# Performance work log

Hardware: AMD Instinct MI355X
Metric: run time of the kernel (lower is better)

## Reference

```python
import jax, jax.numpy as jnp
import numpy as np

B = 64        # number of graphs
NPG = 4096    # nodes per graph (equal-size segments, batch ids sorted)
H = 256       # hidden_dim
C0, C1 = 256, 64  # num_clusters


def setup_inputs() -> dict:
    key = jax.random.key(0)
    ks = jax.random.split(key, 8)
    N = B * NPG
    x = jax.random.normal(ks[0], (N, H), dtype=jnp.float32)
    edge_index = jax.random.randint(ks[1], (2, N), 0, N, dtype=jnp.int64)  # unused by forward
    batch = jnp.repeat(jnp.arange(B, dtype=jnp.int64), NPG)  # sorted, equal-size segments
    s = 1.0 / np.sqrt(H)
    W0 = jax.random.uniform(ks[2], (H, C0), jnp.float32, -s, s)
    b0 = jax.random.uniform(ks[3], (C0,), jnp.float32, -s, s)
    W1 = jax.random.uniform(ks[4], (H, C1), jnp.float32, -s, s)
    b1 = jax.random.uniform(ks[5], (C1,), jnp.float32, -s, s)
    sf = 1.0 / np.sqrt(C1 * H)
    Wf = jax.random.uniform(ks[6], (C1 * H, H), jnp.float32, -sf, sf)
    bf = jax.random.uniform(ks[7], (H,), jnp.float32, -sf, sf)
    return {"x": x, "edge_index": edge_index, "batch": batch,
            "W0": W0, "b0": b0, "W1": W1, "b1": b1, "Wf": Wf, "bf": bf}


def reference(x, edge_index, batch, W0, b0, W1, b1, Wf, bf):
    # Level 0: softmax cluster assignment + per-graph segmented matmul A^T @ F.
    # batch ids are sorted with equal-size segments, so the per-graph Python
    # loop of the original collapses to a reshape + batched einsum.
    A0 = jax.nn.softmax(x @ W0 + b0, axis=-1)                      # [N, C0]
    f0 = jnp.einsum('bnc,bnh->bch',
                    A0.reshape(B, NPG, C0),
                    x.reshape(B, NPG, H)).reshape(B * C0, H)        # [B*C0, H]
    # Level 1: same pattern on pooled cluster features (C0 'nodes' per graph).
    A1 = jax.nn.softmax(f0 @ W1 + b1, axis=-1)                     # [B*C0, C1]
    f1 = jnp.einsum('bnc,bnh->bch',
                    A1.reshape(B, C0, C1),
                    f0.reshape(B, C0, H)).reshape(B, C1 * H)        # [B, C1*H]
    # Final pool: Linear -> ReLU (Dropout is identity in eval mode).
    return jax.nn.relu(f1 @ Wf + bf)                               # [B, H]
```

## Files before the change

kernel.cpp:

```cpp
#include <hip/hip_runtime.h>
#include <stdint.h>

#define NG   64
#define NPG  4096
#define HD   256
#define NC0  256
#define NC1  64

typedef __attribute__((ext_vector_type(8))) short bfx8;
typedef __attribute__((ext_vector_type(4))) float fx4;

__device__ __forceinline__ unsigned short f2bf(float f) {
  union { float f; unsigned int u; } v; v.f = f;
  return (unsigned short)((v.u + 0x7FFFu + ((v.u >> 16) & 1u)) >> 16);
}
__device__ __forceinline__ unsigned int pack2(float a, float b) {
  return (unsigned int)f2bf(a) | ((unsigned int)f2bf(b) << 16);
}

#define ASYNC_COPY16(gptr, lptr) \
  __builtin_amdgcn_global_load_lds((const __attribute__((address_space(1))) unsigned int*)(gptr), \
                                   (__attribute__((address_space(3))) unsigned int*)(lptr), 16, 0, 0)

__global__ __launch_bounds__(256) void k_w0f(const float* __restrict__ W0,
                                             unsigned short* __restrict__ W0F) {
  int gid = blockIdx.x * 256 + threadIdx.x;
  int l15 = gid & 15;
  int q   = (gid >> 4) & 3;
  int ks  = (gid >> 6) & 1;
  int kc  = (gid >> 7) & 3;
  int cblk = gid >> 9;
  int c = cblk * 16 + l15;
  int kb = kc * 64 + ks * 32 + q * 8;
  unsigned int u[4];
  #pragma unroll
  for (int j = 0; j < 8; j += 2)
    u[j >> 1] = pack2(W0[(size_t)(kb + j) * 256 + c], W0[(size_t)(kb + j + 1) * 256 + c]);
  *(float4*)(W0F + (size_t)gid * 8) = *(float4*)u;
}

#define XSP 72
__global__ __launch_bounds__(512, 2) void k_assign0(
    const float* __restrict__ x, const unsigned short* __restrict__ W0F,
    const float* __restrict__ b0, unsigned short* __restrict__ A0T,
    unsigned short* __restrict__ xT, int g0) {
  __shared__ unsigned short xs[2][128 * XSP];
  __shared__ float red[128 * 4];
  unsigned short* at = (unsigned short*)xs;

  int gl = blockIdx.x >> 5, nt = blockIdx.x & 31;
  int tid = threadIdx.x;
  int wave = tid >> 6, lane = tid & 63;
  int wm = wave >> 2, wn = wave & 3;
  int l15 = lane & 15, q = lane >> 4;

  fx4 acc[4][4];
  #pragma unroll
  for (int i = 0; i < 4; ++i)
    #pragma unroll
    for (int j = 0; j < 4; ++j) acc[i][j] = fx4{0.f, 0.f, 0.f, 0.f};

  const float* xbase = x + ((size_t)(g0 + gl) * NPG + (size_t)nt * 128) * HD;
  int snode = tid >> 2, sseg = (tid & 3) * 16;

  bfx8 bvc[4], bvn[4];
  #pragma unroll
  for (int ni = 0; ni < 4; ++ni)
    bvc[ni] = *(const bfx8*)(W0F + ((size_t)(((wn * 4 + ni) * 8 + 0) * 64 + lane)) * 8);

  {
    const float4* src = (const float4*)(xbase + (size_t)snode * HD + sseg);
    float4 v0 = src[0], v1 = src[1], v2 = src[2], v3 = src[3];
    float4 pv[2]; unsigned int* pu = (unsigned int*)pv;
    pu[0] = pack2(v0.x, v0.y); pu[1] = pack2(v0.z, v0.w);
    pu[2] = pack2(v1.x, v1.y); pu[3] = pack2(v1.z, v1.w);
    pu[4] = pack2(v2.x, v2.y); pu[5] = pack2(v2.z, v2.w);
    pu[6] = pack2(v3.x, v3.y); pu[7] = pack2(v3.z, v3.w);
    float4* d = (float4*)&xs[0][snode * XSP + sseg];
    d[0] = pv[0]; d[1] = pv[1];
  }
  __syncthreads();

  for (int kc = 0; kc < 4; ++kc) {
    int buf = kc & 1;
    float4 v0, v1, v2, v3;
    if (kc < 3) {
      const float4* src = (const float4*)(xbase + (size_t)snode * HD + (kc + 1) * 64 + sseg);
      v0 = src[0]; v1 = src[1]; v2 = src[2]; v3 = src[3];
    }
    #pragma unroll
    for (int ks = 0; ks < 2; ++ks) {
      int g8 = kc * 2 + ks;
      if (g8 < 7) {
        #pragma unroll
        for (int ni = 0; ni < 4; ++ni)
          bvn[ni] = *(const bfx8*)(W0F + ((size_t)(((wn * 4 + ni) * 8 + g8 + 1) * 64 + lane)) * 8);
      }
      int kk = ks * 32 + q * 8;
      bfx8 af[4];
      #pragma unroll
      for (int mi = 0; mi < 4; ++mi)
        af[mi] = *(const bfx8*)&xs[buf][(wm * 64 + mi * 16 + l15) * XSP + kk];
      #pragma unroll
      for (int ni = 0; ni < 4; ++ni)
        #pragma unroll
        for (int mi = 0; mi < 4; ++mi)
          acc[mi][ni] = __builtin_amdgcn_mfma_f32_16x16x32_bf16(af[mi], bvc[ni], acc[mi][ni], 0, 0, 0);
      if (g8 < 7) {
        #pragma unroll
        for (int ni = 0; ni < 4; ++ni) bvc[ni] = bvn[ni];
      }
    }
    {
      int hl = tid >> 3;
      int seg = (tid & 7) * 16;
      unsigned int u[8];
      #pragma unroll
      for (int i = 0; i < 16; i += 2) {
        unsigned short a = xs[buf][(seg + i) * XSP + hl];
        unsigned short b = xs[buf][(seg + i + 1) * XSP + hl];
        u[i >> 1] = (unsigned int)a | ((unsigned int)b << 16);
      }
      float4* dst = (float4*)(xT + ((size_t)gl * HD + kc * 64 + hl) * NPG + (size_t)nt * 128 + seg);
      dst[0] = *(float4*)&u[0];
      dst[1] = *(float4*)&u[4];
    }
    if (kc < 3) {
      float4 pv[2]; unsigned int* pu = (unsigned int*)pv;
      pu[0] = pack2(v0.x, v0.y); pu[1] = pack2(v0.z, v0.w);
      pu[2] = pack2(v1.x, v1.y); pu[3] = pack2(v1.z, v1.w);
      pu[4] = pack2(v2.x, v2.y); pu[5] = pack2(v2.z, v2.w);
      pu[6] = pack2(v3.x, v3.y); pu[7] = pack2(v3.z, v3.w);
      float4* d = (float4*)&xs[buf ^ 1][snode * XSP + sseg];
      d[0] = pv[0]; d[1] = pv[1];
    }
    __syncthreads();
  }

  float bv4[4];
  #pragma unroll
  for (int ni = 0; ni < 4; ++ni) bv4[ni] = b0[wn * 64 + ni * 16 + l15];
  #pragma unroll
  for (int mi = 0; mi < 4; ++mi)
    #pragma unroll
    for (int ni = 0; ni < 4; ++ni)
      #pragma unroll
      for (int r = 0; r < 4; ++r) acc[mi][ni][r] += bv4[ni];

  float mrow[4][4];
  #pragma unroll
  for (int mi = 0; mi < 4; ++mi)
    #pragma unroll
    for (int r = 0; r < 4; ++r) {
      float m = fmaxf(fmaxf(acc[mi][0][r], acc[mi][1][r]), fmaxf(acc[mi][2][r], acc[mi][3][r]));
      #pragma unroll
      for (int off = 1; off < 16; off <<= 1) m = fmaxf(m, __shfl_xor(m, off));
      mrow[mi][r] = m;
    }
  if (l15 == 0) {
    #pragma unroll
    for (int mi = 0; mi < 4; ++mi)
      #pragma unroll
      for (int r = 0; r < 4; ++r)
        red[(wm * 64 + mi * 16 + q * 4 + r) * 4 + wn] = mrow[mi][r];
  }
  __syncthreads();
  #pragma unroll
  for (int mi = 0; mi < 4; ++mi)
    #pragma unroll
    for (int r = 0; r < 4; ++r) {
      float4 rv = *(const float4*)&red[(wm * 64 + mi * 16 + q * 4 + r) * 4];
      mrow[mi][r] = fmaxf(fmaxf(rv.x, rv.y), fmaxf(rv.z, rv.w));
    }
  __syncthreads();
  float srow[4][4];
  #pragma unroll
  for (int mi = 0; mi < 4; ++mi)
    #pragma unroll
    for (int r = 0; r < 4; ++r) {
      float s = 0.f;
      #pragma unroll
      for (int ni = 0; ni < 4; ++ni) {
        float e = __expf(acc[mi][ni][r] - mrow[mi][r]);
        acc[mi][ni][r] = e; s += e;
      }
      #pragma unroll
      for (int off = 1; off < 16; off <<= 1) s += __shfl_xor(s, off);
      srow[mi][r] = s;
    }
  if (l15 == 0) {
    #pragma unroll
    for (int mi = 0; mi < 4; ++mi)
      #pragma unroll
      for (int r = 0; r < 4; ++r)
        red[(wm * 64 + mi * 16 + q * 4 + r) * 4 + wn] = srow[mi][r];
  }
  __syncthreads();
  #pragma unroll
  for (int mi = 0; mi < 4; ++mi)
    #pragma unroll
    for (int r = 0; r < 4; ++r) {
      float4 rv = *(const float4*)&red[(wm * 64 + mi * 16 + q * 4 + r) * 4];
      float inv = 1.f / (rv.x + rv.y + rv.z + rv.w);
      #pragma unroll
      for (int ni = 0; ni < 4; ++ni) acc[mi][ni][r] *= inv;
    }
  __syncthreads();

  unsigned short* A0Tg = A0T + (size_t)gl * NC0 * NPG + (size_t)nt * 128;
  #pragma unroll
  for (int p = 0; p < 2; ++p) {
    if ((wn >> 1) == p) {
      int cb = (wn & 1) * 64;
      #pragma unroll
      for (int mi = 0; mi < 4; ++mi) {
        int ncol = wm * 64 + mi * 16 + q * 4;
        #pragma unroll
        for (int ni = 0; ni < 4; ++ni) {
          int cl = cb + ni * 16 + l15;
          uint2 w;
          w.x = pack2(acc[mi][ni][0], acc[mi][ni][1]);
          w.y = pack2(acc[mi][ni][2], acc[mi][ni][3]);
          *(uint2*)(at + cl * 136 + ncol) = w;
        }
      }
    }
    __syncthreads();
    {
      int row = tid >> 2, seg = (tid & 3) * 32;
      const float4* s4 = (const float4*)(at + row * 136 + seg);
      float4 a = s4[0], b = s4[1], c = s4[2], d = s4[3];
      float4* d4 = (float4*)(A0Tg + (size_t)(p * 128 + row) * NPG + seg);
      d4[0] = a; d4[1] = b; d4[2] = c; d4[3] = d;
    }
    __syncthreads();
  }
}

__global__ __launch_bounds__(512, 2) void k_pool0(
    const unsigned short* __restrict__ A0T, const unsigned short* __restrict__ xT,
    float* __restrict__ f0, int g0) {
  __shared__ unsigned short a_s[2][128 * 64];
  __shared__ unsigned short b_s[2][128 * 64];
  int bid = blockIdx.x;
  int nt = bid & 1;
  int mt = (bid >> 1) & 1;
  int gl = bid >> 2;

  int tid = threadIdx.x;
  int wave = tid >> 6, lane = tid & 63;
  int wm = wave >> 2, wn = wave & 3;
  int l15 = lane & 15, q = lane >> 4;

  const unsigned short* abase = A0T + ((size_t)gl * NC0 + (size_t)mt * 128) * NPG;
  const unsigned short* bbase = xT  + ((size_t)gl * HD  + (size_t)nt * 128) * NPG;

  fx4 acc[4][2];
  #pragma unroll
  for (int i = 0; i < 4; ++i)
    #pragma unroll
    for (int j = 0; j < 2; ++j) acc[i][j] = fx4{0.f, 0.f, 0.f, 0.f};

  int srow = lane >> 3;
  int sg   = (lane & 7) ^ srow;
  size_t soff = (size_t)srow * NPG + (size_t)sg * 8;

  #pragma unroll
  for (int i = 0; i < 2; ++i) {
    int r0 = wave * 16 + i * 8;
    ASYNC_COPY16(abase + (size_t)r0 * NPG + soff, &a_s[0][r0 * 64]);
    ASYNC_COPY16(bbase + (size_t)r0 * NPG + soff, &b_s[0][r0 * 64]);
  }
  __syncthreads();

  for (int t = 0; t < NPG / 64; ++t) {
    int buf = t & 1;
    if (t < NPG / 64 - 1) {
      int k0 = (t + 1) * 64;
      #pragma unroll
      for (int i = 0; i < 2; ++i) {
        int r0 = wave * 16 + i * 8;
        ASYNC_COPY16(abase + (size_t)r0 * NPG + k0 + soff, &a_s[buf ^ 1][r0 * 64]);
        ASYNC_COPY16(bbase + (size_t)r0 * NPG + k0 + soff, &b_s[buf ^ 1][r0 * 64]);
      }
    }
    #pragma unroll
    for (int ks = 0; ks < 2; ++ks) {
      int gx = ((ks * 4 + q) ^ (l15 & 7)) << 3;
      bfx8 af[4], bf[2];
      #pragma unroll
      for (int mi = 0; mi < 4; ++mi)
        af[mi] = *(const bfx8*)&a_s[buf][(wm * 64 + mi * 16 + l15) * 64 + gx];
      #pragma unroll
      for (int ni = 0; ni < 2; ++ni)
        bf[ni] = *(const bfx8*)&b_s[buf][(wn * 32 + ni * 16 + l15) * 64 + gx];
      #pragma unroll
      for (int ni = 0; ni < 2; ++ni)
        #pragma unroll
        for (int mi = 0; mi < 4; ++mi)
          acc[mi][ni] = __builtin_amdgcn_mfma_f32_16x16x32_bf16(af[mi], bf[ni], acc[mi][ni], 0, 0, 0);
    }
    __syncthreads();
  }

  float* dst = f0 + ((size_t)(g0 + gl) * NC0 + (size_t)mt * 128) * HD + (size_t)nt * 128;
  #pragma unroll
  for (int mi = 0; mi < 4; ++mi)
    #pragma unroll
    for (int ni = 0; ni < 2; ++ni) {
      int c = wm * 64 + mi * 16 + q * 4;
      int h = wn * 32 + ni * 16 + l15;
      #pragma unroll
      for (int r = 0; r < 4; ++r)
        dst[(size_t)(c + r) * HD + h] = acc[mi][ni][r];
    }
}

__global__ __launch_bounds__(256) void k_assign1(
    const float* __restrict__ f0, const float* __restrict__ W1,
    const float* __restrict__ b1, float* __restrict__ A1) {
  __shared__ float w1s[256 * 64];
  int tid = threadIdx.x;
  #pragma unroll
  for (int i = 0; i < 16; ++i) {
    int off = i * 1024 + tid * 4;
    *(float4*)(w1s + off) = *(const float4*)(W1 + off);
  }
  __syncthreads();
  int lane = tid & 63;
  int rbase = blockIdx.x * 32 + (tid >> 6) * 8;
  float bias = b1[lane];
  for (int rr = 0; rr < 8; ++rr) {
    int row = rbase + rr;
    const float* fr = f0 + (size_t)row * 256;
    float acc = bias;
    for (int k = 0; k < 256; k += 4) {
      float4 fv = *(const float4*)(fr + k);
      acc += fv.x * w1s[(k    ) * 64 + lane];
      acc += fv.y * w1s[(k + 1) * 64 + lane];
      acc += fv.z * w1s[(k + 2) * 64 + lane];
      acc += fv.w * w1s[(k + 3) * 64 + lane];
    }
    float m = acc;
    #pragma unroll
    for (int off = 1; off < 64; off <<= 1) m = fmaxf(m, __shfl_xor(m, off));
    float e = __expf(acc - m);
    float s = e;
    #pragma unroll
    for (int off = 1; off < 64; off <<= 1) s += __shfl_xor(s, off);
    A1[(size_t)row * 64 + lane] = e / s;
  }
}

__global__ __launch_bounds__(256) void k_pool1(
    const float* __restrict__ A1, const float* __restrict__ f0, float* __restrict__ f1) {
  int b = blockIdx.x >> 2, cg = blockIdx.x & 3;
  int h = threadIdx.x;
  const float* a1p = A1 + (size_t)b * NC0 * NC1 + cg * 16;
  const float* f0p = f0 + (size_t)b * NC0 * HD + h;
  float acc[16];
  #pragma unroll
  for (int j = 0; j < 16; ++j) acc[j] = 0.f;
  for (int c0 = 0; c0 < 256; ++c0) {
    float fv = f0p[(size_t)c0 * 256];
    #pragma unroll
    for (int j = 0; j < 16; ++j) acc[j] += a1p[c0 * 64 + j] * fv;
  }
  float* d = f1 + (size_t)b * 16384 + (size_t)(cg * 16) * 256 + h;
  #pragma unroll
  for (int j = 0; j < 16; ++j) d[(size_t)j * 256] = acc[j];
}

__global__ __launch_bounds__(512) void k_final_partial(
    const float* __restrict__ f1, const float* __restrict__ Wf, float* __restrict__ ot) {
  __shared__ float f1s[64 * 256];
  int ht = blockIdx.x & 3;
  int ks = blockIdx.x >> 2;
  int tid = threadIdx.x;
  {
    int b = tid >> 3, c0 = (tid & 7) * 4;
    const float* s = f1 + (size_t)b * 16384 + (size_t)ks * 256 + c0;
    float* d = f1s + b * 256 + c0;
    #pragma unroll
    for (int i = 0; i < 8; ++i) *(float4*)(d + i * 32) = *(const float4*)(s + i * 32);
  }
  __syncthreads();
  int h = ht * 64 + (tid & 63);
  int b0 = (tid >> 6) * 8;
  const float* wp = Wf + (size_t)ks * 256 * 256 + h;
  float acc[8];
  #pragma unroll
  for (int j = 0; j < 8; ++j) acc[j] = 0.f;
  for (int k = 0; k < 256; k += 4) {
    float w0 = wp[(size_t)(k    ) * 256];
    float w1 = wp[(size_t)(k + 1) * 256];
    float w2 = wp[(size_t)(k + 2) * 256];
    float w3 = wp[(size_t)(k + 3) * 256];
    #pragma unroll
    for (int j = 0; j < 8; ++j) {
      float4 fv = *(const float4*)(f1s + (b0 + j) * 256 + k);
      acc[j] += fv.x * w0 + fv.y * w1 + fv.z * w2 + fv.w * w3;
    }
  }
  #pragma unroll
  for (int j = 0; j < 8; ++j) atomicAdd(&ot[(b0 + j) * 256 + h], acc[j]);
}

__global__ __launch_bounds__(256) void k_final_out(
    const float* __restrict__ ot, const float* __restrict__ bfv, float* __restrict__ out) {
  int i = blockIdx.x * 256 + threadIdx.x;
  float v = ot[i] + bfv[i & 255];
  out[i] = v > 0.f ? v : 0.f;
}

extern "C" void kernel_launch(void* const* d_in, const int* in_sizes, int n_in,
                              void* d_out, int out_size, void* d_ws, size_t ws_size,
                              hipStream_t stream) {
  const float* x   = (const float*)d_in[0];
  const float* W0  = (const float*)d_in[3];
  const float* b0  = (const float*)d_in[4];
  const float* W1  = (const float*)d_in[5];
  const float* b1  = (const float*)d_in[6];
  const float* Wf  = (const float*)d_in[7];
  const float* bfv = (const float*)d_in[8];
  float* out = (float*)d_out;
  char* ws = (char*)d_ws;

  float* f0  = (float*)ws;
  float* ot  = (float*)(ws + ((size_t)32 << 20));
  unsigned short* W0F = (unsigned short*)(ws + ((size_t)32 << 20) + 65536);
  size_t chunk_off = ((size_t)32 << 20) + 65536 + 131072;
  size_t per_graph = (size_t)4 * HD * NPG;
  size_t avail = ws_size > chunk_off ? ws_size - chunk_off : 0;
  int G = (int)(avail / per_graph);
  if (G > 64) G = 64;
  if (G < 1) G = 1;
  unsigned short* xT  = (unsigned short*)(ws + chunk_off);
  unsigned short* A0T = xT + (size_t)G * HD * NPG;
  float* f1 = (float*)xT;
  float* A1 = (float*)A0T;

  hipMemsetAsync(ot, 0, 65536, stream);
  k_w0f<<<32, 256, 0, stream>>>(W0, W0F);

  for (int g0 = 0; g0 < NG; g0 += G) {
    int gc = (NG - g0 < G) ? (NG - g0) : G;
    k_assign0<<<gc * 32, 512, 0, stream>>>(x, W0F, b0, A0T, xT, g0);
    k_pool0<<<gc * 4, 512, 0, stream>>>(A0T, xT, f0, g0);
  }
  k_assign1<<<512, 256, 0, stream>>>(f0, W1, b1, A1);
  k_pool1<<<256, 256, 0, stream>>>(A1, f0, f1);
  k_final_partial<<<256, 512, 0, stream>>>(f1, Wf, ot);
  k_final_out<<<64, 256, 0, stream>>>(ot, bfv, out);
}
```

Before: 690.7 us.

## Shrink assign0 tiles to 64 nodes, swizzle LDS, and write tile-contiguous intermediates

k_assign0 now processes 64-node tiles with 256 threads and three blocks per CU, replacing the padded x tile in LDS with an XOR-swizzled layout. The xT and A0T intermediates are stored as contiguous 64-node chunks, so pool0's async loads for each k-step read a contiguous block instead of rows strided by NPG. The aim is higher occupancy, fewer LDS bank conflicts and better DRAM/TLB locality, at the cost of re-reading W0F fragments from more blocks and running twice as many blocks.

```diff
diff --git a/kernel.cpp b/kernel.cpp
--- a/kernel.cpp
+++ b/kernel.cpp
@@ -39,19 +39,16 @@
   *(float4*)(W0F + (size_t)gid * 8) = *(float4*)u;
 }
 
-#define XSP 72
-__global__ __launch_bounds__(512, 2) void k_assign0(
+__global__ __launch_bounds__(256, 3) void k_assign0(
     const float* __restrict__ x, const unsigned short* __restrict__ W0F,
     const float* __restrict__ b0, unsigned short* __restrict__ A0T,
     unsigned short* __restrict__ xT, int g0) {
-  __shared__ unsigned short xs[2][128 * XSP];
-  __shared__ float red[128 * 4];
-  unsigned short* at = (unsigned short*)xs;
-
-  int gl = blockIdx.x >> 5, nt = blockIdx.x & 31;
+  __shared__ unsigned short lds_u[9216];
+  __shared__ float red[64 * 4];
+
+  int gl = blockIdx.x >> 6, nt = blockIdx.x & 63;
   int tid = threadIdx.x;
-  int wave = tid >> 6, lane = tid & 63;
-  int wm = wave >> 2, wn = wave & 3;
+  int wn = tid >> 6, lane = tid & 63;
   int l15 = lane & 15, q = lane >> 4;
 
   fx4 acc[4][4];
@@ -60,8 +57,10 @@
     #pragma unroll
     for (int j = 0; j < 4; ++j) acc[i][j] = fx4{0.f, 0.f, 0.f, 0.f};
 
-  const float* xbase = x + ((size_t)(g0 + gl) * NPG + (size_t)nt * 128) * HD;
+  const float* xbase = x + ((size_t)(g0 + gl) * NPG + (size_t)nt * 64) * HD;
   int snode = tid >> 2, sseg = (tid & 3) * 16;
+  int sg0  = (tid & 3) * 2;
+  int ssw  = (snode ^ (snode >> 4)) & 7;
 
   bfx8 bvc[4], bvn[4];
   #pragma unroll
@@ -76,13 +75,14 @@
     pu[2] = pack2(v1.x, v1.y); pu[3] = pack2(v1.z, v1.w);
     pu[4] = pack2(v2.x, v2.y); pu[5] = pack2(v2.z, v2.w);
     pu[6] = pack2(v3.x, v3.y); pu[7] = pack2(v3.z, v3.w);
-    float4* d = (float4*)&xs[0][snode * XSP + sseg];
-    d[0] = pv[0]; d[1] = pv[1];
+    unsigned short* drow = &lds_u[snode << 6];
+    *(float4*)(drow + (((sg0    ) ^ ssw) << 3)) = pv[0];
+    *(float4*)(drow + (((sg0 + 1) ^ ssw) << 3)) = pv[1];
   }
   __syncthreads();
 
   for (int kc = 0; kc < 4; ++kc) {
-    int buf = kc & 1;
+    const unsigned short* xb = &lds_u[(kc & 1) * 4096];
     float4 v0, v1, v2, v3;
     if (kc < 3) {
       const float4* src = (const float4*)(xbase + (size_t)snode * HD + (kc + 1) * 64 + sseg);
@@ -96,11 +96,13 @@
         for (int ni = 0; ni < 4; ++ni)
           bvn[ni] = *(const bfx8*)(W0F + ((size_t)(((wn * 4 + ni) * 8 + g8 + 1) * 64 + lane)) * 8);
       }
-      int kk = ks * 32 + q * 8;
       bfx8 af[4];
       #pragma unroll
-      for (int mi = 0; mi < 4; ++mi)
-        af[mi] = *(const bfx8*)&xs[buf][(wm * 64 + mi * 16 + l15) * XSP + kk];
+      for (int mi = 0; mi < 4; ++mi) {
+        int row = mi * 16 + l15;
+        int slot = (ks * 4 + q) ^ ((row ^ (row >> 4)) & 7);
+        af[mi] = *(const bfx8*)&xb[(row << 6) + (slot << 3)];
+      }
       #pragma unroll
       for (int ni = 0; ni < 4; ++ni)
         #pragma unroll
@@ -112,16 +114,17 @@
       }
     }
     {
-      int hl = tid >> 3;
-      int seg = (tid & 7) * 16;
+      int hl = tid >> 2, s4 = tid & 3, sgn = s4 * 16;
+      int g = hl >> 3, off = hl & 7;
       unsigned int u[8];
       #pragma unroll
       for (int i = 0; i < 16; i += 2) {
-        unsigned short a = xs[buf][(seg + i) * XSP + hl];
-        unsigned short b = xs[buf][(seg + i + 1) * XSP + hl];
+        int n0 = sgn + i, n1 = n0 + 1;
+        unsigned short a = xb[(n0 << 6) + ((g ^ ((n0 ^ (n0 >> 4)) & 7)) << 3) + off];
+        unsigned short b = xb[(n1 << 6) + ((g ^ ((n1 ^ (n1 >> 4)) & 7)) << 3) + off];
         u[i >> 1] = (unsigned int)a | ((unsigned int)b << 16);
       }
-      float4* dst = (float4*)(xT + ((size_t)gl * HD + kc * 64 + hl) * NPG + (size_t)nt * 128 + seg);
+      float4* dst = (float4*)(xT + ((size_t)(gl * 64 + nt) * HD + kc * 64 + hl) * 64 + sgn);
       dst[0] = *(float4*)&u[0];
       dst[1] = *(float4*)&u[4];
     }
@@ -131,8 +134,9 @@
       pu[2] = pack2(v1.x, v1.y); pu[3] = pack2(v1.z, v1.w);
       pu[4] = pack2(v2.x, v2.y); pu[5] = pack2(v2.z, v2.w);
       pu[6] = pack2(v3.x, v3.y); pu[7] = pack2(v3.z, v3.w);
-      float4* d = (float4*)&xs[buf ^ 1][snode * XSP + sseg];
-      d[0] = pv[0]; d[1] = pv[1];
+      unsigned short* drow = &lds_u[(((kc & 1) ^ 1) * 4096) + (snode << 6)];
+      *(float4*)(drow + (((sg0    ) ^ ssw) << 3)) = pv[0];
+      *(float4*)(drow + (((sg0 + 1) ^ ssw) << 3)) = pv[1];
     }
     __syncthreads();
   }
@@ -162,14 +166,14 @@
     for (int mi = 0; mi < 4; ++mi)
       #pragma unroll
       for (int r = 0; r < 4; ++r)
-        red[(wm * 64 + mi * 16 + q * 4 + r) * 4 + wn] = mrow[mi][r];
+        red[(mi * 16 + q * 4 + r) * 4 + wn] = mrow[mi][r];
   }
   __syncthreads();
   #pragma unroll
   for (int mi = 0; mi < 4; ++mi)
     #pragma unroll
     for (int r = 0; r < 4; ++r) {
-      float4 rv = *(const float4*)&red[(wm * 64 + mi * 16 + q * 4 + r) * 4];
+      float4 rv = *(const float4*)&red[(mi * 16 + q * 4 + r) * 4];
       mrow[mi][r] = fmaxf(fmaxf(rv.x, rv.y), fmaxf(rv.z, rv.w));
     }
   __syncthreads();
@@ -193,44 +197,45 @@
     for (int mi = 0; mi < 4; ++mi)
       #pragma unroll
       for (int r = 0; r < 4; ++r)
-        red[(wm * 64 + mi * 16 + q * 4 + r) * 4 + wn] = srow[mi][r];
+        red[(mi * 16 + q * 4 + r) * 4 + wn] = srow[mi][r];
   }
   __syncthreads();
   #pragma unroll
   for (int mi = 0; mi < 4; ++mi)
     #pragma unroll
     for (int r = 0; r < 4; ++r) {
-      float4 rv = *(const float4*)&red[(wm * 64 + mi * 16 + q * 4 + r) * 4];
+      float4 rv = *(const float4*)&red[(mi * 16 + q * 4 + r) * 4];
       float inv = 1.f / (rv.x + rv.y + rv.z + rv.w);
       #pragma unroll
       for (int ni = 0; ni < 4; ++ni) acc[mi][ni][r] *= inv;
     }
   __syncthreads();
 
-  unsigned short* A0Tg = A0T + (size_t)gl * NC0 * NPG + (size_t)nt * 128;
+  unsigned short* at = lds_u;
+  unsigned short* A0Tg = A0T + (size_t)(gl * 64 + nt) * NC0 * 64;
   #pragma unroll
   for (int p = 0; p < 2; ++p) {
     if ((wn >> 1) == p) {
       int cb = (wn & 1) * 64;
       #pragma unroll
       for (int mi = 0; mi < 4; ++mi) {
-        int ncol = wm * 64 + mi * 16 + q * 4;
+        int ncol = mi * 16 + q * 4;
         #pragma unroll
         for (int ni = 0; ni < 4; ++ni) {
           int cl = cb + ni * 16 + l15;
           uint2 w;
           w.x = pack2(acc[mi][ni][0], acc[mi][ni][1]);
           w.y = pack2(acc[mi][ni][2], acc[mi][ni][3]);
-          *(uint2*)(at + cl * 136 + ncol) = w;
+          *(uint2*)(at + cl * 72 + ncol) = w;
         }
       }
     }
     __syncthreads();
     {
-      int row = tid >> 2, seg = (tid & 3) * 32;
-      const float4* s4 = (const float4*)(at + row * 136 + seg);
-      float4 a = s4[0], b = s4[1], c = s4[2], d = s4[3];
-      float4* d4 = (float4*)(A0Tg + (size_t)(p * 128 + row) * NPG + seg);
+      int row = tid >> 1, sg2 = (tid & 1) * 32;
+      const float4* s4p = (const float4*)(at + row * 72 + sg2);
+      float4 a = s4p[0], b = s4p[1], c = s4p[2], d = s4p[3];
+      float4* d4 = (float4*)(A0Tg + (size_t)(p * 128 + row) * 64 + sg2);
       d4[0] = a; d4[1] = b; d4[2] = c; d4[3] = d;
     }
     __syncthreads();
@@ -252,8 +257,8 @@
   int wm = wave >> 2, wn = wave & 3;
   int l15 = lane & 15, q = lane >> 4;
 
-  const unsigned short* abase = A0T + ((size_t)gl * NC0 + (size_t)mt * 128) * NPG;
-  const unsigned short* bbase = xT  + ((size_t)gl * HD  + (size_t)nt * 128) * NPG;
+  const unsigned short* abase = A0T + (size_t)gl * 64 * NC0 * 64 + (size_t)mt * 128 * 64;
+  const unsigned short* bbase = xT  + (size_t)gl * 64 * HD  * 64 + (size_t)nt * 128 * 64;
 
   fx4 acc[4][2];
   #pragma unroll
@@ -263,25 +268,25 @@
 
   int srow = lane >> 3;
   int sg   = (lane & 7) ^ srow;
-  size_t soff = (size_t)srow * NPG + (size_t)sg * 8;
+  size_t soff = (size_t)srow * 64 + (size_t)sg * 8;
 
   #pragma unroll
   for (int i = 0; i < 2; ++i) {
     int r0 = wave * 16 + i * 8;
-    ASYNC_COPY16(abase + (size_t)r0 * NPG + soff, &a_s[0][r0 * 64]);
-    ASYNC_COPY16(bbase + (size_t)r0 * NPG + soff, &b_s[0][r0 * 64]);
+    ASYNC_COPY16(abase + (size_t)r0 * 64 + soff, &a_s[0][r0 * 64]);
+    ASYNC_COPY16(bbase + (size_t)r0 * 64 + soff, &b_s[0][r0 * 64]);
   }
   __syncthreads();
 
   for (int t = 0; t < NPG / 64; ++t) {
     int buf = t & 1;
     if (t < NPG / 64 - 1) {
-      int k0 = (t + 1) * 64;
+      size_t co = (size_t)(t + 1) * NC0 * 64;
       #pragma unroll
       for (int i = 0; i < 2; ++i) {
         int r0 = wave * 16 + i * 8;
-        ASYNC_COPY16(abase + (size_t)r0 * NPG + k0 + soff, &a_s[buf ^ 1][r0 * 64]);
-        ASYNC_COPY16(bbase + (size_t)r0 * NPG + k0 + soff, &b_s[buf ^ 1][r0 * 64]);
+        ASYNC_COPY16(abase + co + (size_t)r0 * 64 + soff, &a_s[buf ^ 1][r0 * 64]);
+        ASYNC_COPY16(bbase + co + (size_t)r0 * 64 + soff, &b_s[buf ^ 1][r0 * 64]);
       }
     }
     #pragma unroll
@@ -445,7 +450,7 @@
 
   for (int g0 = 0; g0 < NG; g0 += G) {
     int gc = (NG - g0 < G) ? (NG - g0) : G;
-    k_assign0<<<gc * 32, 512, 0, stream>>>(x, W0F, b0, A0T, xT, g0);
+    k_assign0<<<gc * 64, 256, 0, stream>>>(x, W0F, b0, A0T, xT, g0);
     k_pool0<<<gc * 4, 512, 0, stream>>>(A0T, xT, f0, g0);
   }
   k_assign1<<<512, 256, 0, stream>>>(f0, W1, b1, A1);
```

After: 653.2 us. 1.06x faster.
